# Optimization experiments

Hardware: AMD Instinct MI355X
Metric: run time of the kernel (lower is better)

The kernel has to match this reference:

```python
import jax, jax.numpy as jnp
import numpy as np

DIM = 2048
NUM_LADDERS = 3
DEPTH = 5
EPS = 0.01


def setup_inputs() -> dict:
    key = jax.random.key(0)
    ks = jax.random.split(key, 5)
    s = 1.0 / np.sqrt(DIM)
    x = jax.random.normal(ks[0], (4, 2048, DIM), dtype=jnp.float32)
    U_w = jax.random.uniform(ks[1], (DIM, DIM), jnp.float32, -s, s)          # U.weight  [out,in]
    gate_w = jax.random.uniform(ks[2], (DIM, DIM), jnp.float32, -s, s)       # gate_proj.weight
    ladder_w = jax.random.uniform(ks[3], (NUM_LADDERS, DEPTH + 1, DIM), jnp.float32, -s, s)
    V_w = jax.random.uniform(ks[4], (DIM, NUM_LADDERS), jnp.float32, -1.0 / np.sqrt(NUM_LADDERS), 1.0 / np.sqrt(NUM_LADDERS))
    return {"x": x, "U_w": U_w, "gate_w": gate_w, "ladder_w": ladder_w, "V_w": V_w}


def _continued_fraction(a_cf, eps):
    # a_cf: (..., depth). Evaluate a_1/(1 + a_2/(1 + ... a_d/1)) with
    # epsilon-guarded denominators (pole avoidance).
    d = a_cf.shape[-1]
    f = jnp.zeros(a_cf.shape[:-1], a_cf.dtype)
    for k in reversed(range(d)):  # tiny fixed depth: loop is fine
        denom = 1.0 + f
        denom = jnp.where(jnp.abs(denom) < eps,
                          jnp.where(denom >= 0, eps, -eps), denom)
        f = a_cf[..., k] / denom
    return f


def reference(x, U_w, gate_w, ladder_w, V_w):
    linear_out = jnp.einsum('bsd,od->bso', x, U_w)                 # U(x)
    gated_x = jax.nn.sigmoid(jnp.einsum('bsd,od->bso', x, gate_w)) * x
    # All ladders at once: (b,s,L,depth+1)
    a = jnp.einsum('bsd,lkd->bslk', gated_x, ladder_w)
    a0 = a[..., 0]                                                 # (b,s,L)
    z = a0 + _continued_fraction(a[..., 1:], EPS)                  # (b,s,L)
    combined = jnp.einsum('bsl,dl->bsd', z, V_w)                   # V(z)
    return linear_out + combined
```

## Files before the change

### kernel.cpp

```cpp
#include <hip/hip_runtime.h>
#include <cstdint>
#include <cstddef>

#define DIM 2048
#define NROWS 8192
#define NL 3
#define DEPTH 5
#define NLK 18
#define NCB 16
#define CF_EPS 0.01f

typedef __attribute__((ext_vector_type(8))) __bf16 bfrag;
typedef __attribute__((ext_vector_type(4))) float f32x4;

typedef __attribute__((address_space(1))) void gvoid;
typedef __attribute__((address_space(3))) void lvoid;

__device__ __forceinline__ void gld_lds16(const void* g, void* l) {
    __builtin_amdgcn_global_load_lds((gvoid*)g, (lvoid*)l, 16, 0, 0);
}

__global__ __launch_bounds__(256) void mfma_gemm_u(
    const ushort* __restrict__ A, const ushort* __restrict__ B,
    const float* __restrict__ zb, const float* __restrict__ Vp,
    float* __restrict__ C)
{
    constexpr int BK = 32;
    __shared__ __align__(16) ushort sA[128 * BK];
    __shared__ __align__(16) ushort sB[128 * BK];

    const int tid  = threadIdx.x;
    const int wave = tid >> 6;
    const int lane = tid & 63;
    const int wm   = wave & 1;
    const int wn   = wave >> 1;
    const int m0   = blockIdx.y * 128;
    const int n0   = blockIdx.x * 128;

    const size_t soff = (size_t)(wave * 32 + (lane >> 2)) * DIM + (lane & 3) * 8;
    const ushort* gA = A + (size_t)m0 * DIM + soff;
    const ushort* gB = B + (size_t)n0 * DIM + soff;

    ushort* lA0 = &sA[(wave * 32) * BK];
    ushort* lA1 = &sA[(wave * 32 + 16) * BK];
    ushort* lB0 = &sB[(wave * 32) * BK];
    ushort* lB1 = &sB[(wave * 32 + 16) * BK];

    const int fm = lane & 15;
    const int fq = lane >> 4;

    f32x4 acc[4][4];
    #pragma unroll
    for (int i = 0; i < 4; ++i)
        #pragma unroll
        for (int j = 0; j < 4; ++j)
            acc[i][j] = (f32x4){0.f, 0.f, 0.f, 0.f};

    for (int k0 = 0; k0 < DIM; k0 += BK) {
        __syncthreads();
        gld_lds16(gA + k0, lA0);
        gld_lds16(gA + (size_t)16 * DIM + k0, lA1);
        gld_lds16(gB + k0, lB0);
        gld_lds16(gB + (size_t)16 * DIM + k0, lB1);
        __syncthreads();

        bfrag ah[4], bh[4];
        #pragma unroll
        for (int i = 0; i < 4; ++i) {
            ah[i] = *(const bfrag*)&sA[(wm * 64 + i * 16 + fm) * BK + fq * 8];
            bh[i] = *(const bfrag*)&sB[(wn * 64 + i * 16 + fm) * BK + fq * 8];
        }
        #pragma unroll
        for (int i = 0; i < 4; ++i)
            #pragma unroll
            for (int j = 0; j < 4; ++j)
                acc[i][j] = __builtin_amdgcn_mfma_f32_16x16x32_bf16(ah[i], bh[j], acc[i][j], 0, 0, 0);
    }

    float4 vc[4];
    #pragma unroll
    for (int j = 0; j < 4; ++j)
        vc[j] = *(const float4*)&Vp[(size_t)(n0 + wn * 64 + j * 16 + fm) * 4];

    #pragma unroll
    for (int i = 0; i < 4; ++i) {
        const int rowb = m0 + wm * 64 + i * 16 + fq * 4;
        #pragma unroll
        for (int r = 0; r < 4; ++r) {
            const float4 zr = *(const float4*)&zb[(size_t)(rowb + r) * 4];
            #pragma unroll
            for (int j = 0; j < 4; ++j) {
                const int col = n0 + wn * 64 + j * 16 + fm;
                C[(size_t)(rowb + r) * DIM + col] =
                    acc[i][j][r] + zr.x * vc[j].x + zr.y * vc[j].y + zr.z * vc[j].z;
            }
        }
    }
}

__global__ __launch_bounds__(256) void mfma_gemm_gate(
    const ushort* __restrict__ Ah, const ushort* __restrict__ Al,
    const ushort* __restrict__ Bh, const ushort* __restrict__ Bl,
    const float* __restrict__ X,  const float* __restrict__ Lw,
    float* __restrict__ a_part)
{
    constexpr int BK = 32;
    __shared__ __align__(16) char smem[32768];
    ushort* sAh = (ushort*)(smem);
    ushort* sBh = (ushort*)(smem + 8192);
    ushort* sAl = (ushort*)(smem + 16384);
    ushort* sBl = (ushort*)(smem + 24576);
    float*  sG  = (float*)(smem);
    float*  sLw = (float*)(smem + 16896);

    const int tid  = threadIdx.x;
    const int wave = tid >> 6;
    const int lane = tid & 63;
    const int wm   = wave & 1;
    const int wn   = wave >> 1;
    const int m0   = blockIdx.y * 128;
    const int n0   = blockIdx.x * 128;

    const size_t soff = (size_t)(wave * 32 + (lane >> 2)) * DIM + (lane & 3) * 8;
    const ushort* gA  = Ah + (size_t)m0 * DIM + soff;
    const ushort* gAl = Al + (size_t)m0 * DIM + soff;
    const ushort* gB  = Bh + (size_t)n0 * DIM + soff;
    const ushort* gBl = Bl + (size_t)n0 * DIM + soff;

    ushort* lA0  = &sAh[(wave * 32) * BK];
    ushort* lA1  = &sAh[(wave * 32 + 16) * BK];
    ushort* lB0  = &sBh[(wave * 32) * BK];
    ushort* lB1  = &sBh[(wave * 32 + 16) * BK];
    ushort* lAl0 = &sAl[(wave * 32) * BK];
    ushort* lAl1 = &sAl[(wave * 32 + 16) * BK];
    ushort* lBl0 = &sBl[(wave * 32) * BK];
    ushort* lBl1 = &sBl[(wave * 32 + 16) * BK];

    const int fm = lane & 15;
    const int fq = lane >> 4;

    f32x4 acc[4][4];
    #pragma unroll
    for (int i = 0; i < 4; ++i)
        #pragma unroll
        for (int j = 0; j < 4; ++j)
            acc[i][j] = (f32x4){0.f, 0.f, 0.f, 0.f};

    for (int k0 = 0; k0 < DIM; k0 += BK) {
        __syncthreads();
        gld_lds16(gA + k0, lA0);
        gld_lds16(gA + (size_t)16 * DIM + k0, lA1);
        gld_lds16(gB + k0, lB0);
        gld_lds16(gB + (size_t)16 * DIM + k0, lB1);
        gld_lds16(gAl + k0, lAl0);
        gld_lds16(gAl + (size_t)16 * DIM + k0, lAl1);
        gld_lds16(gBl + k0, lBl0);
        gld_lds16(gBl + (size_t)16 * DIM + k0, lBl1);
        __syncthreads();

        bfrag ah[4], bh[4], al[4], bl[4];
        #pragma unroll
        for (int i = 0; i < 4; ++i) {
            ah[i] = *(const bfrag*)&sAh[(wm * 64 + i * 16 + fm) * BK + fq * 8];
            bh[i] = *(const bfrag*)&sBh[(wn * 64 + i * 16 + fm) * BK + fq * 8];
            al[i] = *(const bfrag*)&sAl[(wm * 64 + i * 16 + fm) * BK + fq * 8];
            bl[i] = *(const bfrag*)&sBl[(wn * 64 + i * 16 + fm) * BK + fq * 8];
        }
        #pragma unroll
        for (int i = 0; i < 4; ++i)
            #pragma unroll
            for (int j = 0; j < 4; ++j) {
                acc[i][j] = __builtin_amdgcn_mfma_f32_16x16x32_bf16(ah[i], bh[j], acc[i][j], 0, 0, 0);
                acc[i][j] = __builtin_amdgcn_mfma_f32_16x16x32_bf16(ah[i], bl[j], acc[i][j], 0, 0, 0);
                acc[i][j] = __builtin_amdgcn_mfma_f32_16x16x32_bf16(al[i], bh[j], acc[i][j], 0, 0, 0);
            }
    }

    const float* xblk = X + (size_t)m0 * DIM + n0;
    const int rred  = ((tid >> 6) << 3) | (tid & 7);
    const int strip = (lane >> 3) & 7;
    const int qc    = strip * 16;

#define DO_QUARTER(Q)                                                          \
    {                                                                          \
        __syncthreads();     \
        if (Q == 0) {                                                          \
              \
            for (int idx = tid; idx < NLK * 128; idx += 256) {                 \
                const int lk = idx >> 7, c = idx & 127;                        \
                sLw[lk * 156 + c + ((c >> 4) << 2)] = Lw[(size_t)lk * DIM + n0 + c]; \
            }                                                                  \
        }                                                                      \
        if (wm == (Q >> 1)) {                                                  \
            constexpr int ib = (Q & 1) * 2;   \
            _Pragma("unroll")                                                  \
            for (int ii = 0; ii < 2; ++ii) {                                   \
                _Pragma("unroll")                                              \
                for (int r = 0; r < 4; ++r) {                                  \
                    const int rloc = ii * 16 + fq * 4 + r;          \
                    const float* xr = xblk + (size_t)(Q * 32 + rloc) * DIM;    \
                    _Pragma("unroll")                                          \
                    for (int j = 0; j < 4; ++j) {                              \
                        const int cc = wn * 64 + j * 16 + fm;                  \
                        const float g = acc[ib + ii][j][r];                    \
                        const float s = 1.0f / (1.0f + __expf(-g));            \
                        sG[rloc * 132 + cc] = s * xr[cc];                      \
                    }                                                          \
                }                                                              \
            }                                                                  \
        }                                                                      \
        __syncthreads();                         \
        float p[NLK];                                                          \
        _Pragma("unroll")                                                      \
        for (int lk = 0; lk < NLK; ++lk) p[lk] = 0.f;                          \
        _Pragma("unroll")                                                      \
        for (int c4 = 0; c4 < 16; c4 += 4) {                                   \
            const float4 g4 = *(const float4*)&sG[rred * 132 + qc + c4];       \
            _Pragma("unroll")                                                  \
            for (int lk = 0; lk < NLK; ++lk) {                                 \
                const float4 w4 = *(const float4*)&sLw[lk * 156 + qc + c4 + (strip << 2)]; \
                p[lk] = fmaf(g4.x, w4.x, fmaf(g4.y, w4.y,                      \
                        fmaf(g4.z, w4.z, fmaf(g4.w, w4.w, p[lk]))));           \
            }                                                                  \
        }                                                                      \
        _Pragma("unroll")                                                      \
        for (int lk = 0; lk < NLK; ++lk) {                                     \
            p[lk] += __shfl_xor(p[lk], 8, 64);                                 \
            p[lk] += __shfl_xor(p[lk], 16, 64);                                \
            p[lk] += __shfl_xor(p[lk], 32, 64);                                \
        }                                                                      \
        if ((lane >> 3) == 0) {                                                \
            float* dst = a_part +                                              \
                ((size_t)(m0 + Q * 32 + rred) * NCB + blockIdx.x) * NLK;       \
            _Pragma("unroll")                                                  \
            for (int lk = 0; lk < NLK; ++lk) dst[lk] = p[lk];                  \
        }                                                                      \
    }

    DO_QUARTER(0)
    DO_QUARTER(1)
    DO_QUARTER(2)
    DO_QUARTER(3)
#undef DO_QUARTER
}

__global__ __launch_bounds__(256) void cf_kernel(const float* __restrict__ a_part,
                                                 float* __restrict__ zb)
{
    const int r = blockIdx.x * 256 + threadIdx.x;
    const float* ap = a_part + (size_t)r * NCB * NLK;
    float a[NLK];
    #pragma unroll
    for (int lk = 0; lk < NLK; ++lk) a[lk] = 0.f;
    #pragma unroll 4
    for (int cb = 0; cb < NCB; ++cb) {
        #pragma unroll
        for (int lk = 0; lk < NLK; ++lk)
            a[lk] += ap[cb * NLK + lk];
    }
    float z[NL];
    #pragma unroll
    for (int l = 0; l < NL; ++l) {
        float f = 0.f;
        #pragma unroll
        for (int k = DEPTH - 1; k >= 0; --k) {
            float denom = 1.f + f;
            if (fabsf(denom) < CF_EPS) denom = (denom >= 0.f) ? CF_EPS : -CF_EPS;
            f = a[l * (DEPTH + 1) + k + 1] / denom;
        }
        z[l] = a[l * (DEPTH + 1)] + f;
    }
    *(float4*)&zb[(size_t)r * 4] = make_float4(z[0], z[1], z[2], 0.f);
}

__global__ __launch_bounds__(256) void padV(const float* __restrict__ Vw,
                                            float* __restrict__ Vp)
{
    const int d = blockIdx.x * 256 + threadIdx.x;
    *(float4*)&Vp[(size_t)d * 4] =
        make_float4(Vw[(size_t)d * 3], Vw[(size_t)d * 3 + 1], Vw[(size_t)d * 3 + 2], 0.f);
}

__device__ __forceinline__ ushort f2bf_bits(float f) {
    __bf16 h = (__bf16)f;
    return __builtin_bit_cast(unsigned short, h);
}
__device__ __forceinline__ float bfbits2f(ushort u) {
    __bf16 h = __builtin_bit_cast(__bf16, u);
    return (float)h;
}

union U16x8 { ushort u[8]; uint4 v; };

__global__ __launch_bounds__(256) void split2(const float* __restrict__ src,
                                              ushort* __restrict__ hi,
                                              ushort* __restrict__ lo)
{
    const size_t i0 = ((size_t)blockIdx.x * 256 + threadIdx.x) * 8;
    const float4 v0 = *(const float4*)(src + i0);
    const float4 v1 = *(const float4*)(src + i0 + 4);
    const float f[8] = {v0.x, v0.y, v0.z, v0.w, v1.x, v1.y, v1.z, v1.w};
    U16x8 h, l;
    #pragma unroll
    for (int j = 0; j < 8; ++j) {
        const ushort hb = f2bf_bits(f[j]);
        h.u[j] = hb;
        l.u[j] = f2bf_bits(f[j] - bfbits2f(hb));
    }
    *(uint4*)(hi + i0) = h.v;
    *(uint4*)(lo + i0) = l.v;
}

__global__ __launch_bounds__(256) void tobf16(const float* __restrict__ src,
                                              ushort* __restrict__ dst)
{
    const size_t i0 = ((size_t)blockIdx.x * 256 + threadIdx.x) * 8;
    const float4 v0 = *(const float4*)(src + i0);
    const float4 v1 = *(const float4*)(src + i0 + 4);
    const float f[8] = {v0.x, v0.y, v0.z, v0.w, v1.x, v1.y, v1.z, v1.w};
    U16x8 h;
    #pragma unroll
    for (int j = 0; j < 8; ++j) h.u[j] = f2bf_bits(f[j]);
    *(uint4*)(dst + i0) = h.v;
}

#define BMF 128
#define BNF 128
#define BKF 16
#define LDAF 132

__global__ __launch_bounds__(256) void sgemm_dual(
    const float* __restrict__ X,
    const float* __restrict__ Uw,
    const float* __restrict__ Gw,
    float* __restrict__ outLin,
    float* __restrict__ outGate)
{
    __shared__ float As[BKF][LDAF];
    __shared__ float Bs[BKF][LDAF];

    const int tid = threadIdx.x;
    const int n0 = blockIdx.x * BNF;
    const int m0 = blockIdx.y * BMF;
    const bool isGate = (n0 >= DIM);
    const float* W = isGate ? Gw : Uw;
    float* C = isGate ? outGate : outLin;
    const int nb = isGate ? (n0 - DIM) : n0;

    const int lr = tid >> 2;
    const int lc = (tid & 3) << 2;

    const float* pa0 = X + (size_t)(m0 + lr) * DIM + lc;
    const float* pa1 = X + (size_t)(m0 + lr + 64) * DIM + lc;
    const float* pb0 = W + (size_t)(nb + lr) * DIM + lc;
    const float* pb1 = W + (size_t)(nb + lr + 64) * DIM + lc;

    const int tx = tid & 15;
    const int ty = tid >> 4;

    float acc[8][8];
    #pragma unroll
    for (int i = 0; i < 8; ++i)
        #pragma unroll
        for (int j = 0; j < 8; ++j) acc[i][j] = 0.f;

    for (int k0 = 0; k0 < DIM; k0 += BKF) {
        const float4 a0 = *(const float4*)(pa0 + k0);
        const float4 a1 = *(const float4*)(pa1 + k0);
        const float4 b0 = *(const float4*)(pb0 + k0);
        const float4 b1 = *(const float4*)(pb1 + k0);
        __syncthreads();
        As[lc + 0][lr] = a0.x; As[lc + 1][lr] = a0.y; As[lc + 2][lr] = a0.z; As[lc + 3][lr] = a0.w;
        As[lc + 0][lr + 64] = a1.x; As[lc + 1][lr + 64] = a1.y; As[lc + 2][lr + 64] = a1.z; As[lc + 3][lr + 64] = a1.w;
        Bs[lc + 0][lr] = b0.x; Bs[lc + 1][lr] = b0.y; Bs[lc + 2][lr] = b0.z; Bs[lc + 3][lr] = b0.w;
        Bs[lc + 0][lr + 64] = b1.x; Bs[lc + 1][lr + 64] = b1.y; Bs[lc + 2][lr + 64] = b1.z; Bs[lc + 3][lr + 64] = b1.w;
        __syncthreads();
        #pragma unroll
        for (int kk = 0; kk < BKF; ++kk) {
            float av[8], bv[8];
            *(float4*)&av[0] = *(const float4*)&As[kk][ty * 8];
            *(float4*)&av[4] = *(const float4*)&As[kk][ty * 8 + 4];
            *(float4*)&bv[0] = *(const float4*)&Bs[kk][tx * 8];
            *(float4*)&bv[4] = *(const float4*)&Bs[kk][tx * 8 + 4];
            #pragma unroll
            for (int i = 0; i < 8; ++i)
                #pragma unroll
                for (int j = 0; j < 8; ++j)
                    acc[i][j] = fmaf(av[i], bv[j], acc[i][j]);
        }
    }

    #pragma unroll
    for (int i = 0; i < 8; ++i) {
        float* crow = C + (size_t)(m0 + ty * 8 + i) * DIM + nb + tx * 8;
        *(float4*)crow       = make_float4(acc[i][0], acc[i][1], acc[i][2], acc[i][3]);
        *(float4*)(crow + 4) = make_float4(acc[i][4], acc[i][5], acc[i][6], acc[i][7]);
    }
}

__global__ __launch_bounds__(256) void ladder_epilogue(
    const float* __restrict__ X,
    const float* __restrict__ G,
    const float* __restrict__ Lw,
    const float* __restrict__ Vw,
    float* __restrict__ Out)
{
    const int r = blockIdx.x;
    const int tid = threadIdx.x;
    const int d0 = tid * 8;
    const float* xrow = X + (size_t)r * DIM;
    const float* grow = G + (size_t)r * DIM;

    const float4 xv0 = *(const float4*)(xrow + d0);
    const float4 xv1 = *(const float4*)(xrow + d0 + 4);
    const float4 gv0 = *(const float4*)(grow + d0);
    const float4 gv1 = *(const float4*)(grow + d0 + 4);

    float gated[8];
    {
        const float gx[8] = {gv0.x, gv0.y, gv0.z, gv0.w, gv1.x, gv1.y, gv1.z, gv1.w};
        const float xx[8] = {xv0.x, xv0.y, xv0.z, xv0.w, xv1.x, xv1.y, xv1.z, xv1.w};
        #pragma unroll
        for (int j = 0; j < 8; ++j) {
            const float s = 1.0f / (1.0f + __expf(-gx[j]));
            gated[j] = s * xx[j];
        }
    }

    float part[NLK];
    #pragma unroll
    for (int lk = 0; lk < NLK; ++lk) {
        const float* lrow = Lw + (size_t)lk * DIM + d0;
        const float4 w0 = *(const float4*)lrow;
        const float4 w1 = *(const float4*)(lrow + 4);
        part[lk] = gated[0] * w0.x + gated[1] * w0.y + gated[2] * w0.z + gated[3] * w0.w
                 + gated[4] * w1.x + gated[5] * w1.y + gated[6] * w1.z + gated[7] * w1.w;
    }

    #pragma unroll
    for (int off = 32; off > 0; off >>= 1) {
        #pragma unroll
        for (int lk = 0; lk < NLK; ++lk)
            part[lk] += __shfl_down(part[lk], off, 64);
    }

    __shared__ float red[4][NLK];
    __shared__ float zsh[NL];
    const int wave = tid >> 6;
    const int lane = tid & 63;
    if (lane == 0) {
        #pragma unroll
        for (int lk = 0; lk < NLK; ++lk) red[wave][lk] = part[lk];
    }
    __syncthreads();
    if (tid < NL) {
        float a[DEPTH + 1];
        #pragma unroll
        for (int k = 0; k < DEPTH + 1; ++k)
            a[k] = red[0][tid * 6 + k] + red[1][tid * 6 + k]
                 + red[2][tid * 6 + k] + red[3][tid * 6 + k];
        float f = 0.f;
        #pragma unroll
        for (int k = DEPTH - 1; k >= 0; --k) {
            float denom = 1.f + f;
            if (fabsf(denom) < CF_EPS) denom = (denom >= 0.f) ? CF_EPS : -CF_EPS;
            f = a[k + 1] / denom;
        }
        zsh[tid] = a[0] + f;
    }
    __syncthreads();
    const float z0 = zsh[0], z1 = zsh[1], z2 = zsh[2];

    float* orow = Out + (size_t)r * DIM + d0;
    const float4 o0 = *(const float4*)orow;
    const float4 o1 = *(const float4*)(orow + 4);
    float ov[8] = {o0.x, o0.y, o0.z, o0.w, o1.x, o1.y, o1.z, o1.w};
    #pragma unroll
    for (int j = 0; j < 8; ++j) {
        const float* vp = Vw + (size_t)(d0 + j) * NL;
        ov[j] += z0 * vp[0] + z1 * vp[1] + z2 * vp[2];
    }
    *(float4*)orow       = make_float4(ov[0], ov[1], ov[2], ov[3]);
    *(float4*)(orow + 4) = make_float4(ov[4], ov[5], ov[6], ov[7]);
}

extern "C" void kernel_launch(void* const* d_in, const int* in_sizes, int n_in,
                              void* d_out, int out_size, void* d_ws, size_t ws_size,
                              hipStream_t stream) {
    const float* X  = (const float*)d_in[0];
    const float* Uw = (const float*)d_in[1];
    const float* Gw = (const float*)d_in[2];
    const float* Lw = (const float*)d_in[3];
    const float* Vw = (const float*)d_in[4];
    float* out = (float*)d_out;

    const size_t WS_NEED = 101875712ull;
    char* ws = (char*)d_ws;

    if (ws_size >= WS_NEED) {
        ushort* Xh     = (ushort*)(ws);
        ushort* Xl     = (ushort*)(ws + 33554432);
        ushort* Gwh    = (ushort*)(ws + 67108864);
        ushort* Gwl    = (ushort*)(ws + 75497472);
        ushort* Uwh    = (ushort*)(ws + 83886080);
        float*  a_part = (float*)(ws + 92274688);
        float*  z_buf  = (float*)(ws + 101711872);
        float*  Vp     = (float*)(ws + 101842944);

        split2<<<dim3(8192), dim3(256), 0, stream>>>(X, Xh, Xl);
        split2<<<dim3(2048), dim3(256), 0, stream>>>(Gw, Gwh, Gwl);
        tobf16<<<dim3(2048), dim3(256), 0, stream>>>(Uw, Uwh);
        padV  <<<dim3(8),    dim3(256), 0, stream>>>(Vw, Vp);

        dim3 grid(DIM / 128, NROWS / 128);
        mfma_gemm_gate<<<grid, dim3(256), 0, stream>>>(Xh, Xl, Gwh, Gwl, X, Lw, a_part);
        cf_kernel<<<dim3(32), dim3(256), 0, stream>>>(a_part, z_buf);
        mfma_gemm_u<<<grid, dim3(256), 0, stream>>>(Xh, Uwh, z_buf, Vp, out);
    } else {
        float* gbuf = (float*)ws;
        dim3 grid(2 * DIM / BNF, NROWS / BMF);
        sgemm_dual<<<grid, dim3(256), 0, stream>>>(X, Uw, Gw, out, gbuf);
        ladder_epilogue<<<dim3(NROWS), dim3(256), 0, stream>>>(X, gbuf, Lw, Vw, out);
    }
}
```

Measured before the change: 488.4 us.

## Fuse gate and U GEMMs into one kernel sharing X tiles, add z·V in epilogue pass

The gate GEMM (3-pass bf16 split) and the U GEMM (1-pass bf16) now run in one kernel that loads the X hi/lo tiles once and keeps two accumulator sets. The U result is written straight to the output, and a new per-row kernel reduces the ladder partials, evaluates the continued fraction, and adds z·V to the output in place. This removes one full re-read of X and one GEMM launch. In exchange it doubles accumulator registers, which may lower occupancy, and it adds an extra read-modify-write pass over the 64MB output.

```diff
diff --git a/kernel.cpp b/kernel.cpp
--- a/kernel.cpp
+++ b/kernel.cpp
@@ -20,14 +20,22 @@
     __builtin_amdgcn_global_load_lds((gvoid*)g, (lvoid*)l, 16, 0, 0);
 }
 
-__global__ __launch_bounds__(256) void mfma_gemm_u(
-    const ushort* __restrict__ A, const ushort* __restrict__ B,
-    const float* __restrict__ zb, const float* __restrict__ Vp,
-    float* __restrict__ C)
+__global__ __launch_bounds__(256) void mfma_gemm_fused(
+    const ushort* __restrict__ Xh, const ushort* __restrict__ Xl,
+    const ushort* __restrict__ Gwh, const ushort* __restrict__ Gwl,
+    const ushort* __restrict__ Uwh,
+    const float* __restrict__ X,  const float* __restrict__ Lw,
+    float* __restrict__ outU, float* __restrict__ a_part)
 {
     constexpr int BK = 32;
-    __shared__ __align__(16) ushort sA[128 * BK];
-    __shared__ __align__(16) ushort sB[128 * BK];
+    __shared__ __align__(16) char smem[40960];
+    ushort* sXh = (ushort*)(smem);
+    ushort* sXl = (ushort*)(smem + 8192);
+    ushort* sGh = (ushort*)(smem + 16384);
+    ushort* sGl = (ushort*)(smem + 24576);
+    ushort* sUh = (ushort*)(smem + 32768);
+    float*  sG  = (float*)(smem);
+    float*  sLw = (float*)(smem + 16896);
 
     const int tid  = threadIdx.x;
     const int wave = tid >> 6;
@@ -38,142 +46,80 @@
     const int n0   = blockIdx.x * 128;
 
     const size_t soff = (size_t)(wave * 32 + (lane >> 2)) * DIM + (lane & 3) * 8;
-    const ushort* gA = A + (size_t)m0 * DIM + soff;
-    const ushort* gB = B + (size_t)n0 * DIM + soff;
-
-    ushort* lA0 = &sA[(wave * 32) * BK];
-    ushort* lA1 = &sA[(wave * 32 + 16) * BK];
-    ushort* lB0 = &sB[(wave * 32) * BK];
-    ushort* lB1 = &sB[(wave * 32 + 16) * BK];
+    const ushort* gXh = Xh  + (size_t)m0 * DIM + soff;
+    const ushort* gXl = Xl  + (size_t)m0 * DIM + soff;
+    const ushort* gGh = Gwh + (size_t)n0 * DIM + soff;
+    const ushort* gGl = Gwl + (size_t)n0 * DIM + soff;
+    const ushort* gUh = Uwh + (size_t)n0 * DIM + soff;
+
+    ushort* lXh0 = &sXh[(wave * 32) * BK];
+    ushort* lXh1 = &sXh[(wave * 32 + 16) * BK];
+    ushort* lXl0 = &sXl[(wave * 32) * BK];
+    ushort* lXl1 = &sXl[(wave * 32 + 16) * BK];
+    ushort* lGh0 = &sGh[(wave * 32) * BK];
+    ushort* lGh1 = &sGh[(wave * 32 + 16) * BK];
+    ushort* lGl0 = &sGl[(wave * 32) * BK];
+    ushort* lGl1 = &sGl[(wave * 32 + 16) * BK];
+    ushort* lUh0 = &sUh[(wave * 32) * BK];
+    ushort* lUh1 = &sUh[(wave * 32 + 16) * BK];
 
     const int fm = lane & 15;
     const int fq = lane >> 4;
 
-    f32x4 acc[4][4];
+    f32x4 accG[4][4], accU[4][4];
     #pragma unroll
     for (int i = 0; i < 4; ++i)
         #pragma unroll
-        for (int j = 0; j < 4; ++j)
-            acc[i][j] = (f32x4){0.f, 0.f, 0.f, 0.f};
+        for (int j = 0; j < 4; ++j) {
+            accG[i][j] = (f32x4){0.f, 0.f, 0.f, 0.f};
+            accU[i][j] = (f32x4){0.f, 0.f, 0.f, 0.f};
+        }
 
     for (int k0 = 0; k0 < DIM; k0 += BK) {
         __syncthreads();
-        gld_lds16(gA + k0, lA0);
-        gld_lds16(gA + (size_t)16 * DIM + k0, lA1);
-        gld_lds16(gB + k0, lB0);
-        gld_lds16(gB + (size_t)16 * DIM + k0, lB1);
+        gld_lds16(gXh + k0, lXh0);
+        gld_lds16(gXh + (size_t)16 * DIM + k0, lXh1);
+        gld_lds16(gXl + k0, lXl0);
+        gld_lds16(gXl + (size_t)16 * DIM + k0, lXl1);
+        gld_lds16(gGh + k0, lGh0);
+        gld_lds16(gGh + (size_t)16 * DIM + k0, lGh1);
+        gld_lds16(gGl + k0, lGl0);
+        gld_lds16(gGl + (size_t)16 * DIM + k0, lGl1);
+        gld_lds16(gUh + k0, lUh0);
+        gld_lds16(gUh + (size_t)16 * DIM + k0, lUh1);
         __syncthreads();
 
-        bfrag ah[4], bh[4];
+        bfrag ah[4], al[4];
         #pragma unroll
         for (int i = 0; i < 4; ++i) {
-            ah[i] = *(const bfrag*)&sA[(wm * 64 + i * 16 + fm) * BK + fq * 8];
-            bh[i] = *(const bfrag*)&sB[(wn * 64 + i * 16 + fm) * BK + fq * 8];
-        }
-        #pragma unroll
-        for (int i = 0; i < 4; ++i)
+            ah[i] = *(const bfrag*)&sXh[(wm * 64 + i * 16 + fm) * BK + fq * 8];
+            al[i] = *(const bfrag*)&sXl[(wm * 64 + i * 16 + fm) * BK + fq * 8];
+        }
+        #pragma unroll
+        for (int j = 0; j < 4; ++j) {
+            const bfrag bh = *(const bfrag*)&sGh[(wn * 64 + j * 16 + fm) * BK + fq * 8];
+            const bfrag bl = *(const bfrag*)&sGl[(wn * 64 + j * 16 + fm) * BK + fq * 8];
+            const bfrag bu = *(const bfrag*)&sUh[(wn * 64 + j * 16 + fm) * BK + fq * 8];
             #pragma unroll
-            for (int j = 0; j < 4; ++j)
-                acc[i][j] = __builtin_amdgcn_mfma_f32_16x16x32_bf16(ah[i], bh[j], acc[i][j], 0, 0, 0);
-    }
-
-    float4 vc[4];
-    #pragma unroll
-    for (int j = 0; j < 4; ++j)
-        vc[j] = *(const float4*)&Vp[(size_t)(n0 + wn * 64 + j * 16 + fm) * 4];
+            for (int i = 0; i < 4; ++i) {
+                accG[i][j] = __builtin_amdgcn_mfma_f32_16x16x32_bf16(ah[i], bh, accG[i][j], 0, 0, 0);
+                accG[i][j] = __builtin_amdgcn_mfma_f32_16x16x32_bf16(ah[i], bl, accG[i][j], 0, 0, 0);
+                accG[i][j] = __builtin_amdgcn_mfma_f32_16x16x32_bf16(al[i], bh, accG[i][j], 0, 0, 0);
+                accU[i][j] = __builtin_amdgcn_mfma_f32_16x16x32_bf16(ah[i], bu, accU[i][j], 0, 0, 0);
+            }
+        }
+    }
 
     #pragma unroll
     for (int i = 0; i < 4; ++i) {
         const int rowb = m0 + wm * 64 + i * 16 + fq * 4;
         #pragma unroll
-        for (int r = 0; r < 4; ++r) {
-            const float4 zr = *(const float4*)&zb[(size_t)(rowb + r) * 4];
+        for (int j = 0; j < 4; ++j) {
+            const int col = n0 + wn * 64 + j * 16 + fm;
             #pragma unroll
-            for (int j = 0; j < 4; ++j) {
-                const int col = n0 + wn * 64 + j * 16 + fm;
-                C[(size_t)(rowb + r) * DIM + col] =
-                    acc[i][j][r] + zr.x * vc[j].x + zr.y * vc[j].y + zr.z * vc[j].z;
-            }
-        }
-    }
-}
-
-__global__ __launch_bounds__(256) void mfma_gemm_gate(
-    const ushort* __restrict__ Ah, const ushort* __restrict__ Al,
-    const ushort* __restrict__ Bh, const ushort* __restrict__ Bl,
-    const float* __restrict__ X,  const float* __restrict__ Lw,
-    float* __restrict__ a_part)
-{
-    constexpr int BK = 32;
-    __shared__ __align__(16) char smem[32768];
-    ushort* sAh = (ushort*)(smem);
-    ushort* sBh = (ushort*)(smem + 8192);
-    ushort* sAl = (ushort*)(smem + 16384);
-    ushort* sBl = (ushort*)(smem + 24576);
-    float*  sG  = (float*)(smem);
-    float*  sLw = (float*)(smem + 16896);
-
-    const int tid  = threadIdx.x;
-    const int wave = tid >> 6;
-    const int lane = tid & 63;
-    const int wm   = wave & 1;
-    const int wn   = wave >> 1;
-    const int m0   = blockIdx.y * 128;
-    const int n0   = blockIdx.x * 128;
-
-    const size_t soff = (size_t)(wave * 32 + (lane >> 2)) * DIM + (lane & 3) * 8;
-    const ushort* gA  = Ah + (size_t)m0 * DIM + soff;
-    const ushort* gAl = Al + (size_t)m0 * DIM + soff;
-    const ushort* gB  = Bh + (size_t)n0 * DIM + soff;
-    const ushort* gBl = Bl + (size_t)n0 * DIM + soff;
-
-    ushort* lA0  = &sAh[(wave * 32) * BK];
-    ushort* lA1  = &sAh[(wave * 32 + 16) * BK];
-    ushort* lB0  = &sBh[(wave * 32) * BK];
-    ushort* lB1  = &sBh[(wave * 32 + 16) * BK];
-    ushort* lAl0 = &sAl[(wave * 32) * BK];
-    ushort* lAl1 = &sAl[(wave * 32 + 16) * BK];
-    ushort* lBl0 = &sBl[(wave * 32) * BK];
-    ushort* lBl1 = &sBl[(wave * 32 + 16) * BK];
-
-    const int fm = lane & 15;
-    const int fq = lane >> 4;
-
-    f32x4 acc[4][4];
-    #pragma unroll
-    for (int i = 0; i < 4; ++i)
-        #pragma unroll
-        for (int j = 0; j < 4; ++j)
-            acc[i][j] = (f32x4){0.f, 0.f, 0.f, 0.f};
-
-    for (int k0 = 0; k0 < DIM; k0 += BK) {
-        __syncthreads();
-        gld_lds16(gA + k0, lA0);
-        gld_lds16(gA + (size_t)16 * DIM + k0, lA1);
-        gld_lds16(gB + k0, lB0);
-        gld_lds16(gB + (size_t)16 * DIM + k0, lB1);
-        gld_lds16(gAl + k0, lAl0);
-        gld_lds16(gAl + (size_t)16 * DIM + k0, lAl1);
-        gld_lds16(gBl + k0, lBl0);
-        gld_lds16(gBl + (size_t)16 * DIM + k0, lBl1);
-        __syncthreads();
-
-        bfrag ah[4], bh[4], al[4], bl[4];
-        #pragma unroll
-        for (int i = 0; i < 4; ++i) {
-            ah[i] = *(const bfrag*)&sAh[(wm * 64 + i * 16 + fm) * BK + fq * 8];
-            bh[i] = *(const bfrag*)&sBh[(wn * 64 + i * 16 + fm) * BK + fq * 8];
-            al[i] = *(const bfrag*)&sAl[(wm * 64 + i * 16 + fm) * BK + fq * 8];
-            bl[i] = *(const bfrag*)&sBl[(wn * 64 + i * 16 + fm) * BK + fq * 8];
-        }
-        #pragma unroll
-        for (int i = 0; i < 4; ++i)
-            #pragma unroll
-            for (int j = 0; j < 4; ++j) {
-                acc[i][j] = __builtin_amdgcn_mfma_f32_16x16x32_bf16(ah[i], bh[j], acc[i][j], 0, 0, 0);
-                acc[i][j] = __builtin_amdgcn_mfma_f32_16x16x32_bf16(ah[i], bl[j], acc[i][j], 0, 0, 0);
-                acc[i][j] = __builtin_amdgcn_mfma_f32_16x16x32_bf16(al[i], bh[j], acc[i][j], 0, 0, 0);
-            }
+            for (int r = 0; r < 4; ++r)
+                outU[(size_t)(rowb + r) * DIM + col] = accU[i][j][r];
+        }
     }
 
     const float* xblk = X + (size_t)m0 * DIM + n0;
@@ -202,7 +148,7 @@
                     _Pragma("unroll")                                          \
                     for (int j = 0; j < 4; ++j) {                              \
                         const int cc = wn * 64 + j * 16 + fm;                  \
-                        const float g = acc[ib + ii][j][r];                    \
+                        const float g = accG[ib + ii][j][r];                   \
                         const float s = 1.0f / (1.0f + __expf(-g));            \
                         sG[rloc * 132 + cc] = s * xr[cc];                      \
                     }                                                          \
@@ -244,33 +190,48 @@
 #undef DO_QUARTER
 }
 
-__global__ __launch_bounds__(256) void cf_kernel(const float* __restrict__ a_part,
-                                                 float* __restrict__ zb)
-{
-    const int r = blockIdx.x * 256 + threadIdx.x;
-    const float* ap = a_part + (size_t)r * NCB * NLK;
-    float a[NLK];
-    #pragma unroll
-    for (int lk = 0; lk < NLK; ++lk) a[lk] = 0.f;
-    #pragma unroll 4
-    for (int cb = 0; cb < NCB; ++cb) {
-        #pragma unroll
-        for (int lk = 0; lk < NLK; ++lk)
-            a[lk] += ap[cb * NLK + lk];
-    }
-    float z[NL];
-    #pragma unroll
-    for (int l = 0; l < NL; ++l) {
+__global__ __launch_bounds__(256) void zv_cf_add(
+    float* __restrict__ out, const float* __restrict__ a_part,
+    const float* __restrict__ Vp)
+{
+    __shared__ float red[NLK];
+    __shared__ float zsh[NL];
+    const int r = blockIdx.x;
+    const int tid = threadIdx.x;
+
+    if (tid < NLK) {
+        const float* ap = a_part + (size_t)r * NCB * NLK + tid;
+        float s = 0.f;
+        #pragma unroll
+        for (int cb = 0; cb < NCB; ++cb) s += ap[cb * NLK];
+        red[tid] = s;
+    }
+    __syncthreads();
+    if (tid < NL) {
         float f = 0.f;
         #pragma unroll
         for (int k = DEPTH - 1; k >= 0; --k) {
             float denom = 1.f + f;
             if (fabsf(denom) < CF_EPS) denom = (denom >= 0.f) ? CF_EPS : -CF_EPS;
-            f = a[l * (DEPTH + 1) + k + 1] / denom;
-        }
-        z[l] = a[l * (DEPTH + 1)] + f;
-    }
-    *(float4*)&zb[(size_t)r * 4] = make_float4(z[0], z[1], z[2], 0.f);
+            f = red[tid * 6 + k + 1] / denom;
+        }
+        zsh[tid] = red[tid * 6] + f;
+    }
+    __syncthreads();
+    const float z0 = zsh[0], z1 = zsh[1], z2 = zsh[2];
+
+    const int c0 = tid * 8;
+    float* orow = out + (size_t)r * DIM + c0;
+    const float4 o0 = *(const float4*)orow;
+    const float4 o1 = *(const float4*)(orow + 4);
+    float ov[8] = {o0.x, o0.y, o0.z, o0.w, o1.x, o1.y, o1.z, o1.w};
+    #pragma unroll
+    for (int j = 0; j < 8; ++j) {
+        const float4 v = *(const float4*)&Vp[(size_t)(c0 + j) * 4];
+        ov[j] += z0 * v.x + z1 * v.y + z2 * v.z;
+    }
+    *(float4*)orow       = make_float4(ov[0], ov[1], ov[2], ov[3]);
+    *(float4*)(orow + 4) = make_float4(ov[4], ov[5], ov[6], ov[7]);
 }
 
 __global__ __launch_bounds__(256) void padV(const float* __restrict__ Vw,
@@ -494,7 +455,7 @@
     const float* Vw = (const float*)d_in[4];
     float* out = (float*)d_out;
 
-    const size_t WS_NEED = 101875712ull;
+    const size_t WS_NEED = 101744640ull;
     char* ws = (char*)d_ws;
 
     if (ws_size >= WS_NEED) {
@@ -504,8 +465,7 @@
         ushort* Gwl    = (ushort*)(ws + 75497472);
         ushort* Uwh    = (ushort*)(ws + 83886080);
         float*  a_part = (float*)(ws + 92274688);
-        float*  z_buf  = (float*)(ws + 101711872);
-        float*  Vp     = (float*)(ws + 101842944);
+        float*  Vp     = (float*)(ws + 101711872);
 
         split2<<<dim3(8192), dim3(256), 0, stream>>>(X, Xh, Xl);
         split2<<<dim3(2048), dim3(256), 0, stream>>>(Gw, Gwh, Gwl);
@@ -513,9 +473,9 @@
         padV  <<<dim3(8),    dim3(256), 0, stream>>>(Vw, Vp);
 
         dim3 grid(DIM / 128, NROWS / 128);
-        mfma_gemm_gate<<<grid, dim3(256), 0, stream>>>(Xh, Xl, Gwh, Gwl, X, Lw, a_part);
-        cf_kernel<<<dim3(32), dim3(256), 0, stream>>>(a_part, z_buf);
-        mfma_gemm_u<<<grid, dim3(256), 0, stream>>>(Xh, Uwh, z_buf, Vp, out);
+        mfma_gemm_fused<<<grid, dim3(256), 0, stream>>>(Xh, Xl, Gwh, Gwl, Uwh,
+                                                        X, Lw, out, a_part);
+        zv_cf_add<<<dim3(NROWS), dim3(256), 0, stream>>>(out, a_part, Vp);
     } else {
         float* gbuf = (float*)ws;
         dim3 grid(2 * DIM / BNF, NROWS / BMF);
```

Result: slower. 696.5 us (+42.6%).

## Double-buffer LDS tiles in both bf16 MFMA GEMM main loops

Applied to the files above, without the earlier changes.

Both GEMM kernels now keep two LDS buffers and issue the async global-to-LDS loads for tile t+1 before computing on tile t. This replaces the old pattern of two barriers per K step, where loads and MFMA work ran strictly one after the other. The aim is to overlap global memory latency with matrix-core work and drop one barrier per iteration. In exchange, LDS use doubles (64KB in the gate kernel), which can lower the number of blocks resident per CU.

```diff
diff --git a/kernel.cpp b/kernel.cpp
--- a/kernel.cpp
+++ b/kernel.cpp
@@ -26,8 +26,10 @@
     float* __restrict__ C)
 {
     constexpr int BK = 32;
-    __shared__ __align__(16) ushort sA[128 * BK];
-    __shared__ __align__(16) ushort sB[128 * BK];
+    constexpr int NT = DIM / BK;
+    constexpr int TILE_E = 128 * BK;
+    constexpr int BUF_E  = 2 * TILE_E;
+    __shared__ __align__(16) ushort smem_u[2 * BUF_E];
 
     const int tid  = threadIdx.x;
     const int wave = tid >> 6;
@@ -41,10 +43,17 @@
     const ushort* gA = A + (size_t)m0 * DIM + soff;
     const ushort* gB = B + (size_t)n0 * DIM + soff;
 
-    ushort* lA0 = &sA[(wave * 32) * BK];
-    ushort* lA1 = &sA[(wave * 32 + 16) * BK];
-    ushort* lB0 = &sB[(wave * 32) * BK];
-    ushort* lB1 = &sB[(wave * 32 + 16) * BK];
+    const int st0 = (wave * 32) * BK;
+    const int st1 = (wave * 32 + 16) * BK;
+
+#define STAGE_U(K0S, BSEL)                                                     \
+    {                                                                          \
+        ushort* bp = smem_u + (BSEL) * BUF_E;                                  \
+        gld_lds16(gA + (K0S), bp + st0);                                       \
+        gld_lds16(gA + (size_t)16 * DIM + (K0S), bp + st1);                    \
+        gld_lds16(gB + (K0S), bp + TILE_E + st0);                              \
+        gld_lds16(gB + (size_t)16 * DIM + (K0S), bp + TILE_E + st1);           \
+    }
 
     const int fm = lane & 15;
     const int fq = lane >> 4;
@@ -56,26 +65,30 @@
         for (int j = 0; j < 4; ++j)
             acc[i][j] = (f32x4){0.f, 0.f, 0.f, 0.f};
 
-    for (int k0 = 0; k0 < DIM; k0 += BK) {
-        __syncthreads();
-        gld_lds16(gA + k0, lA0);
-        gld_lds16(gA + (size_t)16 * DIM + k0, lA1);
-        gld_lds16(gB + k0, lB0);
-        gld_lds16(gB + (size_t)16 * DIM + k0, lB1);
-        __syncthreads();
-
+    STAGE_U(0, 0)
+    __syncthreads();
+
+    for (int t = 0; t < NT; ++t) {
+        if (t + 1 < NT) STAGE_U((t + 1) * BK, (t + 1) & 1)
+
+        const ushort* bp = smem_u + (t & 1) * BUF_E;
+        const ushort* pA = bp;
+        const ushort* pB = bp + TILE_E;
         bfrag ah[4], bh[4];
         #pragma unroll
         for (int i = 0; i < 4; ++i) {
-            ah[i] = *(const bfrag*)&sA[(wm * 64 + i * 16 + fm) * BK + fq * 8];
-            bh[i] = *(const bfrag*)&sB[(wn * 64 + i * 16 + fm) * BK + fq * 8];
+            ah[i] = *(const bfrag*)&pA[(wm * 64 + i * 16 + fm) * BK + fq * 8];
+            bh[i] = *(const bfrag*)&pB[(wn * 64 + i * 16 + fm) * BK + fq * 8];
         }
         #pragma unroll
         for (int i = 0; i < 4; ++i)
             #pragma unroll
             for (int j = 0; j < 4; ++j)
                 acc[i][j] = __builtin_amdgcn_mfma_f32_16x16x32_bf16(ah[i], bh[j], acc[i][j], 0, 0, 0);
-    }
+
+        __syncthreads();
+    }
+#undef STAGE_U
 
     float4 vc[4];
     #pragma unroll
@@ -105,13 +118,12 @@
     float* __restrict__ a_part)
 {
     constexpr int BK = 32;
-    __shared__ __align__(16) char smem[32768];
-    ushort* sAh = (ushort*)(smem);
-    ushort* sBh = (ushort*)(smem + 8192);
-    ushort* sAl = (ushort*)(smem + 16384);
-    ushort* sBl = (ushort*)(smem + 24576);
-    float*  sG  = (float*)(smem);
-    float*  sLw = (float*)(smem + 16896);
+    constexpr int NT = DIM / BK;
+    constexpr int TILE_E = 128 * BK;
+    constexpr int BUF_E  = 4 * TILE_E;
+    __shared__ __align__(16) ushort smem_u[2 * BUF_E];
+    float*  sG  = (float*)smem_u;
+    float*  sLw = (float*)((char*)smem_u + 16896);
 
     const int tid  = threadIdx.x;
     const int wave = tid >> 6;
@@ -127,14 +139,21 @@
     const ushort* gB  = Bh + (size_t)n0 * DIM + soff;
     const ushort* gBl = Bl + (size_t)n0 * DIM + soff;
 
-    ushort* lA0  = &sAh[(wave * 32) * BK];
-    ushort* lA1  = &sAh[(wave * 32 + 16) * BK];
-    ushort* lB0  = &sBh[(wave * 32) * BK];
-    ushort* lB1  = &sBh[(wave * 32 + 16) * BK];
-    ushort* lAl0 = &sAl[(wave * 32) * BK];
-    ushort* lAl1 = &sAl[(wave * 32 + 16) * BK];
-    ushort* lBl0 = &sBl[(wave * 32) * BK];
-    ushort* lBl1 = &sBl[(wave * 32 + 16) * BK];
+    const int st0 = (wave * 32) * BK;
+    const int st1 = (wave * 32 + 16) * BK;
+
+#define STAGE_G(K0S, BSEL)                                                     \
+    {                                                                          \
+        ushort* bp = smem_u + (BSEL) * BUF_E;                                  \
+        gld_lds16(gA  + (K0S), bp + st0);                                      \
+        gld_lds16(gA  + (size_t)16 * DIM + (K0S), bp + st1);                   \
+        gld_lds16(gB  + (K0S), bp + TILE_E + st0);                             \
+        gld_lds16(gB  + (size_t)16 * DIM + (K0S), bp + TILE_E + st1);          \
+        gld_lds16(gAl + (K0S), bp + 2 * TILE_E + st0);                         \
+        gld_lds16(gAl + (size_t)16 * DIM + (K0S), bp + 2 * TILE_E + st1);      \
+        gld_lds16(gBl + (K0S), bp + 3 * TILE_E + st0);                         \
+        gld_lds16(gBl + (size_t)16 * DIM + (K0S), bp + 3 * TILE_E + st1);      \
+    }
 
     const int fm = lane & 15;
     const int fq = lane >> 4;
@@ -146,25 +165,25 @@
         for (int j = 0; j < 4; ++j)
             acc[i][j] = (f32x4){0.f, 0.f, 0.f, 0.f};
 
-    for (int k0 = 0; k0 < DIM; k0 += BK) {
-        __syncthreads();
-        gld_lds16(gA + k0, lA0);
-        gld_lds16(gA + (size_t)16 * DIM + k0, lA1);
-        gld_lds16(gB + k0, lB0);
-        gld_lds16(gB + (size_t)16 * DIM + k0, lB1);
-        gld_lds16(gAl + k0, lAl0);
-        gld_lds16(gAl + (size_t)16 * DIM + k0, lAl1);
-        gld_lds16(gBl + k0, lBl0);
-        gld_lds16(gBl + (size_t)16 * DIM + k0, lBl1);
-        __syncthreads();
+    STAGE_G(0, 0)
+    __syncthreads();
+
+    for (int t = 0; t < NT; ++t) {
+        if (t + 1 < NT) STAGE_G((t + 1) * BK, (t + 1) & 1)
+
+        const ushort* bp  = smem_u + (t & 1) * BUF_E;
+        const ushort* bAh = bp;
+        const ushort* bBh = bp + TILE_E;
+        const ushort* bAl = bp + 2 * TILE_E;
+        const ushort* bBl = bp + 3 * TILE_E;
 
         bfrag ah[4], bh[4], al[4], bl[4];
         #pragma unroll
         for (int i = 0; i < 4; ++i) {
-            ah[i] = *(const bfrag*)&sAh[(wm * 64 + i * 16 + fm) * BK + fq * 8];
-            bh[i] = *(const bfrag*)&sBh[(wn * 64 + i * 16 + fm) * BK + fq * 8];
-            al[i] = *(const bfrag*)&sAl[(wm * 64 + i * 16 + fm) * BK + fq * 8];
-            bl[i] = *(const bfrag*)&sBl[(wn * 64 + i * 16 + fm) * BK + fq * 8];
+            ah[i] = *(const bfrag*)&bAh[(wm * 64 + i * 16 + fm) * BK + fq * 8];
+            bh[i] = *(const bfrag*)&bBh[(wn * 64 + i * 16 + fm) * BK + fq * 8];
+            al[i] = *(const bfrag*)&bAl[(wm * 64 + i * 16 + fm) * BK + fq * 8];
+            bl[i] = *(const bfrag*)&bBl[(wn * 64 + i * 16 + fm) * BK + fq * 8];
         }
         #pragma unroll
         for (int i = 0; i < 4; ++i)
@@ -174,7 +193,10 @@
                 acc[i][j] = __builtin_amdgcn_mfma_f32_16x16x32_bf16(ah[i], bl[j], acc[i][j], 0, 0, 0);
                 acc[i][j] = __builtin_amdgcn_mfma_f32_16x16x32_bf16(al[i], bh[j], acc[i][j], 0, 0, 0);
             }
-    }
+
+        __syncthreads();
+    }
+#undef STAGE_G
 
     const float* xblk = X + (size_t)m0 * DIM + n0;
     const int rred  = ((tid >> 6) << 3) | (tid & 7);
@@ -183,7 +205,7 @@
 
 #define DO_QUARTER(Q)                                                          \
     {                                                                          \
-        __syncthreads();     \
+        __syncthreads();                      \
         if (Q == 0) {                                                          \
               \
             for (int idx = tid; idx < NLK * 128; idx += 256) {                 \
```

Result: slower. 507.2 us (+3.8%).
